# Performance work log

Hardware: AMD Instinct MI355X
Metric: run time of the kernel (lower is better)

The kernel has to match this reference:

```python
import math
import jax, jax.numpy as jnp
import numpy as np

NUM_HEADS = 32
KV_HEADS = 8
HEAD_DIM = 128
BLOCK_SIZE = 16
MAX_CTX = 2048
BSZ = 64
BLOCKS_PER_SEQ = MAX_CTX // BLOCK_SIZE  # 128
NUM_BLOCKS = BSZ * BLOCKS_PER_SEQ       # 8192


def setup_inputs() -> dict:
    key = jax.random.key(0)
    k1, k2, k3, k4 = jax.random.split(key, 4)
    query = jax.random.normal(k1, (BSZ, NUM_HEADS, HEAD_DIM), dtype=jnp.float32)
    key_cache = jax.random.normal(k2, (NUM_BLOCKS, KV_HEADS, BLOCK_SIZE, HEAD_DIM), dtype=jnp.float32)
    value_cache = jax.random.normal(k3, (NUM_BLOCKS, KV_HEADS, BLOCK_SIZE, HEAD_DIM), dtype=jnp.float32)
    # each sequence owns a contiguous run of blocks (valid paged layout)
    block_tables = jnp.arange(NUM_BLOCKS, dtype=jnp.int32).reshape(BSZ, BLOCKS_PER_SEQ)
    # per-sequence context lengths in [1, MAX_CTX]
    input_lens = jax.random.randint(k4, (BSZ,), 1, MAX_CTX + 1, dtype=jnp.int32)
    return {
        "query": query,
        "key_cache": key_cache,
        "value_cache": value_cache,
        "block_tables": block_tables,
        "input_lens": input_lens,
    }


def reference(query, key_cache, value_cache, block_tables, input_lens):
    """Paged single-query cached-KV attention with GQA (decode path of _IPEXAttention).

    query:       [bsz, num_heads, head_dim]  (one new token per sequence)
    key_cache:   [num_blocks, kv_heads, block_size, head_dim]
    value_cache: [num_blocks, kv_heads, block_size, head_dim]
    block_tables:[bsz, blocks_per_seq] int32
    input_lens:  [bsz] int32 valid context length per sequence
    returns:     [bsz, num_heads * head_dim]
    """
    bsz, nh, hd = query.shape
    groups = nh // KV_HEADS  # kv_head_mapping = arange(KV_HEADS).repeat_interleave(groups)
    scale = 1.0 / math.sqrt(hd)

    # Gather paged KV: [bsz, blocks, kvh, bs, hd] -> [bsz, kvh, S, hd]
    k = key_cache[block_tables].transpose(0, 2, 1, 3, 4).reshape(bsz, KV_HEADS, -1, hd)
    v = value_cache[block_tables].transpose(0, 2, 1, 3, 4).reshape(bsz, KV_HEADS, -1, hd)
    S = k.shape[2]

    # GQA: query heads grouped by their kv head
    q = query.reshape(bsz, KV_HEADS, groups, hd)

    scores = jnp.einsum("bkgd,bksd->bkgs", q, k) * scale  # [bsz, kvh, groups, S]
    valid = jnp.arange(S, dtype=jnp.int32)[None, :] < input_lens[:, None]  # [bsz, S]
    neg = jnp.finfo(scores.dtype).min
    scores = jnp.where(valid[:, None, None, :], scores, neg)
    probs = jax.nn.softmax(scores, axis=-1)

    out = jnp.einsum("bkgs,bksd->bkgd", probs, v)  # [bsz, kvh, groups, hd]
    # attn_output.reshape(-1, num_heads * head_dim) as in the torch module
    return out.reshape(bsz, nh * hd)
```

## Files before the change

### kernel.cpp

```cpp
#include <hip/hip_runtime.h>
#include <math.h>

#define NUM_HEADS 32
#define KV_HEADS 8
#define GROUPS 4
#define HEAD_DIM 128
#define BLOCK_SIZE 16
#define MAX_CTX 2048
#define BSZ 64
#define BLOCKS_PER_SEQ 128

#define CHUNK_BLOCKS 16
#define CHUNK_TOKENS (CHUNK_BLOCKS * BLOCK_SIZE)
#define NCHUNK (MAX_CTX / CHUNK_TOKENS)
#define REC_STRIDE 520

__global__ __launch_bounds__(256, 4)
void attn_partial_kernel(const float* __restrict__ q,
                         const float* __restrict__ kcache,
                         const float* __restrict__ vcache,
                         const int*   __restrict__ btab,
                         const int*   __restrict__ lens,
                         float*       __restrict__ part)
{
    const int chunk = blockIdx.x;
    const int kvh   = blockIdx.y;
    const int seq   = blockIdx.z;

    const int len  = lens[seq];
    const int tok0 = chunk * CHUNK_TOKENS;
    if (tok0 >= len) return;

    const int tid  = threadIdx.x;
    const int wave = tid >> 6;
    const int lane = tid & 63;
    const int half = lane >> 5;
    const int c    = lane & 31;

    const float scale = 0.08838834764831845f;

    float4 qv[GROUPS];
    const float* qbase = q + ((size_t)seq * NUM_HEADS + (size_t)kvh * GROUPS) * HEAD_DIM + c * 4;
#pragma unroll
    for (int h = 0; h < GROUPS; ++h) {
        float4 t = *(const float4*)(qbase + h * HEAD_DIM);
        qv[h] = make_float4(t.x * scale, t.y * scale, t.z * scale, t.w * scale);
    }

    float  m[GROUPS], l[GROUPS];
    float4 o[GROUPS];
#pragma unroll
    for (int h = 0; h < GROUPS; ++h) {
        m[h] = -INFINITY; l[h] = 0.f; o[h] = make_float4(0.f, 0.f, 0.f, 0.f);
    }

    const int nblk   = (len + BLOCK_SIZE - 1) / BLOCK_SIZE;
    const int bstart = chunk * CHUNK_BLOCKS;
    const int bend   = min(bstart + CHUNK_BLOCKS, nblk);

    for (int b = bstart + wave; b < bend; b += 4) {
        const int phys = btab[seq * BLOCKS_PER_SEQ + b];
        const size_t slice = ((size_t)phys * KV_HEADS + kvh) * (BLOCK_SIZE * HEAD_DIM);
        const float* kblk = kcache + slice;
        const float* vblk = vcache + slice;
        const int tbase = b * BLOCK_SIZE;

#pragma unroll
        for (int it = 0; it < 8; ++it) {
            const int off = (it * 64 + lane) * 4;
            float4 k4 = *(const float4*)(kblk + off);
            float4 v4 = *(const float4*)(vblk + off);
            const bool valid = (tbase + 2 * it + half) < len;

            float s[GROUPS];
#pragma unroll
            for (int h = 0; h < GROUPS; ++h) {
                float p = k4.x * qv[h].x + k4.y * qv[h].y + k4.z * qv[h].z + k4.w * qv[h].w;
#pragma unroll
                for (int d = 1; d < 32; d <<= 1)
                    p += __shfl_xor(p, d, 64);
                s[h] = p;
            }

            if (valid) {
#pragma unroll
                for (int h = 0; h < GROUPS; ++h) {
                    float mn    = fmaxf(m[h], s[h]);
                    float alpha = __expf(m[h] - mn);
                    float p     = __expf(s[h] - mn);
                    l[h] = l[h] * alpha + p;
                    o[h].x = o[h].x * alpha + p * v4.x;
                    o[h].y = o[h].y * alpha + p * v4.y;
                    o[h].z = o[h].z * alpha + p * v4.z;
                    o[h].w = o[h].w * alpha + p * v4.w;
                    m[h] = mn;
                }
            }
        }
    }

#pragma unroll
    for (int h = 0; h < GROUPS; ++h) {
        float mo = __shfl_xor(m[h], 32, 64);
        float m2 = fmaxf(m[h], mo);
        float w  = (m[h] == -INFINITY) ? 0.f : __expf(m[h] - m2);
        float ls = l[h] * w;
        l[h] = ls + __shfl_xor(ls, 32, 64);
        o[h].x *= w; o[h].y *= w; o[h].z *= w; o[h].w *= w;
        o[h].x += __shfl_xor(o[h].x, 32, 64);
        o[h].y += __shfl_xor(o[h].y, 32, 64);
        o[h].z += __shfl_xor(o[h].z, 32, 64);
        o[h].w += __shfl_xor(o[h].w, 32, 64);
        m[h] = m2;
    }

    __shared__ float o_lds[4][GROUPS][HEAD_DIM];
    __shared__ float m_lds[4][GROUPS];
    __shared__ float l_lds[4][GROUPS];
    if (half == 0) {
#pragma unroll
        for (int h = 0; h < GROUPS; ++h)
            *(float4*)&o_lds[wave][h][c * 4] = o[h];
        if (c == 0) {
#pragma unroll
            for (int h = 0; h < GROUPS; ++h) { m_lds[wave][h] = m[h]; l_lds[wave][h] = l[h]; }
        }
    }
    __syncthreads();

    float* rec = part + (((size_t)(seq * KV_HEADS + kvh)) * NCHUNK + chunk) * REC_STRIDE;
#pragma unroll
    for (int r = 0; r < 2; ++r) {
        const int e = tid + r * 256;
        const int h = e >> 7;
        const int d = e & 127;
        float mstar = fmaxf(fmaxf(m_lds[0][h], m_lds[1][h]),
                            fmaxf(m_lds[2][h], m_lds[3][h]));
        float num = 0.f, L = 0.f;
#pragma unroll
        for (int w = 0; w < 4; ++w) {
            float mw = m_lds[w][h];
            float ww = (mw == -INFINITY) ? 0.f : __expf(mw - mstar);
            num += o_lds[w][h][d] * ww;
            L   += l_lds[w][h] * ww;
        }
        rec[e] = num;
        if (d == 0) { rec[512 + h] = mstar; rec[516 + h] = L; }
    }
}

__global__ __launch_bounds__(256)
void attn_reduce_kernel(const float* __restrict__ part,
                        const int*   __restrict__ lens,
                        float*       __restrict__ out)
{
    const int kvh = blockIdx.x & (KV_HEADS - 1);
    const int seq = blockIdx.x / KV_HEADS;
    const int len = lens[seq];
    const int nlive = (len + CHUNK_TOKENS - 1) / CHUNK_TOKENS;

    const float* base = part + ((size_t)(seq * KV_HEADS + kvh)) * NCHUNK * REC_STRIDE;
    const int tid = threadIdx.x;

#pragma unroll
    for (int r = 0; r < 2; ++r) {
        const int e = tid + r * 256;
        const int h = e >> 7;
        const int d = e & 127;

        float mstar = -INFINITY;
        for (int ch = 0; ch < nlive; ++ch)
            mstar = fmaxf(mstar, base[ch * REC_STRIDE + 512 + h]);

        float num = 0.f, L = 0.f;
        for (int ch = 0; ch < nlive; ++ch) {
            const float* r0 = base + ch * REC_STRIDE;
            float ww = __expf(r0[512 + h] - mstar);
            num += r0[e] * ww;
            L   += r0[516 + h] * ww;
        }
        out[(size_t)seq * (NUM_HEADS * HEAD_DIM) + (kvh * GROUPS + h) * HEAD_DIM + d] = num / L;
    }
}

extern "C" void kernel_launch(void* const* d_in, const int* in_sizes, int n_in,
                              void* d_out, int out_size, void* d_ws, size_t ws_size,
                              hipStream_t stream) {
    const float* q    = (const float*)d_in[0];
    const float* kc   = (const float*)d_in[1];
    const float* vc   = (const float*)d_in[2];
    const int*   bt   = (const int*)d_in[3];
    const int*   lens = (const int*)d_in[4];
    float* out  = (float*)d_out;
    float* part = (float*)d_ws;

    dim3 g1(NCHUNK, KV_HEADS, BSZ);
    attn_partial_kernel<<<g1, 256, 0, stream>>>(q, kc, vc, bt, lens, part);

    dim3 g2(BSZ * KV_HEADS);
    attn_reduce_kernel<<<g2, 256, 0, stream>>>(part, lens, out);
}
```

Measured before the change: 991.9 us.

## Restructure decode attention per-block: 16-lane token groups, block-wise online softmax, exp2

Each wave now maps 16 lanes per token, with each lane covering 8 dims in two float4 halves, so a 16-token block is processed as 4 tokens per lane group. Shuffle reductions drop from 5 steps to 4 and are batched across 4 tokens and 4 heads. The online softmax rescale happens once per block instead of once per token. The log2e factor is folded into the query scale so exp2f can be used. This raises register pressure (launch bounds lowered to 3 blocks per SM) in exchange for fewer cross-lane ops and exp evaluations.

```diff
diff --git a/kernel.cpp b/kernel.cpp
--- a/kernel.cpp
+++ b/kernel.cpp
@@ -15,7 +15,7 @@
 #define NCHUNK (MAX_CTX / CHUNK_TOKENS)
 #define REC_STRIDE 520
 
-__global__ __launch_bounds__(256, 4)
+__global__ __launch_bounds__(256, 3)
 void attn_partial_kernel(const float* __restrict__ q,
                          const float* __restrict__ kcache,
                          const float* __restrict__ vcache,
@@ -27,31 +27,34 @@
     const int kvh   = blockIdx.y;
     const int seq   = blockIdx.z;
 
-    const int len  = lens[seq];
-    const int tok0 = chunk * CHUNK_TOKENS;
-    if (tok0 >= len) return;
+    const int len = lens[seq];
+    if (chunk * CHUNK_TOKENS >= len) return;
 
     const int tid  = threadIdx.x;
     const int wave = tid >> 6;
     const int lane = tid & 63;
-    const int half = lane >> 5;
-    const int c    = lane & 31;
-
-    const float scale = 0.08838834764831845f;
-
-    float4 qv[GROUPS];
-    const float* qbase = q + ((size_t)seq * NUM_HEADS + (size_t)kvh * GROUPS) * HEAD_DIM + c * 4;
+    const int g    = lane >> 4;
+    const int u    = lane & 15;
+
+    const float qs = 0.08838834764831845f * 1.44269504088896340736f;
+
+    float4 qa[GROUPS], qb[GROUPS];
+    const float* qbase = q + ((size_t)seq * NUM_HEADS + (size_t)kvh * GROUPS) * HEAD_DIM;
 #pragma unroll
     for (int h = 0; h < GROUPS; ++h) {
-        float4 t = *(const float4*)(qbase + h * HEAD_DIM);
-        qv[h] = make_float4(t.x * scale, t.y * scale, t.z * scale, t.w * scale);
+        float4 t = *(const float4*)(qbase + h * HEAD_DIM + 4 * u);
+        qa[h] = make_float4(t.x * qs, t.y * qs, t.z * qs, t.w * qs);
+        t = *(const float4*)(qbase + h * HEAD_DIM + 64 + 4 * u);
+        qb[h] = make_float4(t.x * qs, t.y * qs, t.z * qs, t.w * qs);
     }
 
     float  m[GROUPS], l[GROUPS];
-    float4 o[GROUPS];
+    float4 oa[GROUPS], ob[GROUPS];
 #pragma unroll
     for (int h = 0; h < GROUPS; ++h) {
-        m[h] = -INFINITY; l[h] = 0.f; o[h] = make_float4(0.f, 0.f, 0.f, 0.f);
+        m[h] = -INFINITY; l[h] = 0.f;
+        oa[h] = make_float4(0.f, 0.f, 0.f, 0.f);
+        ob[h] = make_float4(0.f, 0.f, 0.f, 0.f);
     }
 
     const int nblk   = (len + BLOCK_SIZE - 1) / BLOCK_SIZE;
@@ -63,65 +66,101 @@
         const size_t slice = ((size_t)phys * KV_HEADS + kvh) * (BLOCK_SIZE * HEAD_DIM);
         const float* kblk = kcache + slice;
         const float* vblk = vcache + slice;
-        const int tbase = b * BLOCK_SIZE;
-
-#pragma unroll
-        for (int it = 0; it < 8; ++it) {
-            const int off = (it * 64 + lane) * 4;
-            float4 k4 = *(const float4*)(kblk + off);
-            float4 v4 = *(const float4*)(vblk + off);
-            const bool valid = (tbase + 2 * it + half) < len;
-
-            float s[GROUPS];
+
+        float  s[4][GROUPS];
+        float4 va[4], vb[4];
+#pragma unroll
+        for (int j = 0; j < 4; ++j) {
+            const int off = (4 * j + g) * HEAD_DIM + 4 * u;
+            float4 ka = *(const float4*)(kblk + off);
+            float4 kb = *(const float4*)(kblk + off + 64);
+            va[j] = *(const float4*)(vblk + off);
+            vb[j] = *(const float4*)(vblk + off + 64);
 #pragma unroll
             for (int h = 0; h < GROUPS; ++h) {
-                float p = k4.x * qv[h].x + k4.y * qv[h].y + k4.z * qv[h].z + k4.w * qv[h].w;
-#pragma unroll
-                for (int d = 1; d < 32; d <<= 1)
-                    p += __shfl_xor(p, d, 64);
-                s[h] = p;
+                s[j][h] = ka.x * qa[h].x + ka.y * qa[h].y + ka.z * qa[h].z + ka.w * qa[h].w
+                        + kb.x * qb[h].x + kb.y * qb[h].y + kb.z * qb[h].z + kb.w * qb[h].w;
             }
-
-            if (valid) {
-#pragma unroll
-                for (int h = 0; h < GROUPS; ++h) {
-                    float mn    = fmaxf(m[h], s[h]);
-                    float alpha = __expf(m[h] - mn);
-                    float p     = __expf(s[h] - mn);
-                    l[h] = l[h] * alpha + p;
-                    o[h].x = o[h].x * alpha + p * v4.x;
-                    o[h].y = o[h].y * alpha + p * v4.y;
-                    o[h].z = o[h].z * alpha + p * v4.z;
-                    o[h].w = o[h].w * alpha + p * v4.w;
-                    m[h] = mn;
-                }
+        }
+
+#pragma unroll
+        for (int d = 1; d < 16; d <<= 1) {
+#pragma unroll
+            for (int j = 0; j < 4; ++j)
+#pragma unroll
+                for (int h = 0; h < GROUPS; ++h)
+                    s[j][h] += __shfl_xor(s[j][h], d, 64);
+        }
+
+        const int tb = b * BLOCK_SIZE + g;
+#pragma unroll
+        for (int j = 0; j < 4; ++j) {
+            if (tb + 4 * j >= len) {
+#pragma unroll
+                for (int h = 0; h < GROUPS; ++h) s[j][h] = -INFINITY;
             }
         }
-    }
-
-#pragma unroll
-    for (int h = 0; h < GROUPS; ++h) {
-        float mo = __shfl_xor(m[h], 32, 64);
-        float m2 = fmaxf(m[h], mo);
-        float w  = (m[h] == -INFINITY) ? 0.f : __expf(m[h] - m2);
-        float ls = l[h] * w;
-        l[h] = ls + __shfl_xor(ls, 32, 64);
-        o[h].x *= w; o[h].y *= w; o[h].z *= w; o[h].w *= w;
-        o[h].x += __shfl_xor(o[h].x, 32, 64);
-        o[h].y += __shfl_xor(o[h].y, 32, 64);
-        o[h].z += __shfl_xor(o[h].z, 32, 64);
-        o[h].w += __shfl_xor(o[h].w, 32, 64);
-        m[h] = m2;
+
+#pragma unroll
+        for (int h = 0; h < GROUPS; ++h) {
+            float bm = fmaxf(fmaxf(s[0][h], s[1][h]), fmaxf(s[2][h], s[3][h]));
+            bm = fmaxf(bm, __shfl_xor(bm, 16, 64));
+            bm = fmaxf(bm, __shfl_xor(bm, 32, 64));
+            const float mn    = fmaxf(m[h], bm);
+            const float alpha = exp2f(m[h] - mn);
+            l[h] *= alpha;
+            oa[h].x *= alpha; oa[h].y *= alpha; oa[h].z *= alpha; oa[h].w *= alpha;
+            ob[h].x *= alpha; ob[h].y *= alpha; ob[h].z *= alpha; ob[h].w *= alpha;
+            m[h] = mn;
+        }
+
+#pragma unroll
+        for (int j = 0; j < 4; ++j) {
+#pragma unroll
+            for (int h = 0; h < GROUPS; ++h) {
+                const float p = exp2f(s[j][h] - m[h]);
+                l[h] += p;
+                oa[h].x += p * va[j].x; oa[h].y += p * va[j].y;
+                oa[h].z += p * va[j].z; oa[h].w += p * va[j].w;
+                ob[h].x += p * vb[j].x; ob[h].y += p * vb[j].y;
+                ob[h].z += p * vb[j].z; ob[h].w += p * vb[j].w;
+            }
+        }
+    }
+
+#pragma unroll
+    for (int d = 16; d <= 32; d <<= 1) {
+#pragma unroll
+        for (int h = 0; h < GROUPS; ++h) {
+            const float mo = __shfl_xor(m[h], d, 64);
+            const float mn = fmaxf(m[h], mo);
+            const float w  = (m[h] == -INFINITY) ? 0.f : exp2f(m[h] - mn);
+            float ls = l[h] * w;
+            l[h] = ls + __shfl_xor(ls, d, 64);
+            oa[h].x *= w; oa[h].y *= w; oa[h].z *= w; oa[h].w *= w;
+            ob[h].x *= w; ob[h].y *= w; ob[h].z *= w; ob[h].w *= w;
+            oa[h].x += __shfl_xor(oa[h].x, d, 64);
+            oa[h].y += __shfl_xor(oa[h].y, d, 64);
+            oa[h].z += __shfl_xor(oa[h].z, d, 64);
+            oa[h].w += __shfl_xor(oa[h].w, d, 64);
+            ob[h].x += __shfl_xor(ob[h].x, d, 64);
+            ob[h].y += __shfl_xor(ob[h].y, d, 64);
+            ob[h].z += __shfl_xor(ob[h].z, d, 64);
+            ob[h].w += __shfl_xor(ob[h].w, d, 64);
+            m[h] = mn;
+        }
     }
 
     __shared__ float o_lds[4][GROUPS][HEAD_DIM];
     __shared__ float m_lds[4][GROUPS];
     __shared__ float l_lds[4][GROUPS];
-    if (half == 0) {
-#pragma unroll
-        for (int h = 0; h < GROUPS; ++h)
-            *(float4*)&o_lds[wave][h][c * 4] = o[h];
-        if (c == 0) {
+    if (g == 0) {
+#pragma unroll
+        for (int h = 0; h < GROUPS; ++h) {
+            *(float4*)&o_lds[wave][h][4 * u]      = oa[h];
+            *(float4*)&o_lds[wave][h][64 + 4 * u] = ob[h];
+        }
+        if (u == 0) {
 #pragma unroll
             for (int h = 0; h < GROUPS; ++h) { m_lds[wave][h] = m[h]; l_lds[wave][h] = l[h]; }
         }
@@ -140,7 +179,7 @@
 #pragma unroll
         for (int w = 0; w < 4; ++w) {
             float mw = m_lds[w][h];
-            float ww = (mw == -INFINITY) ? 0.f : __expf(mw - mstar);
+            float ww = (mw == -INFINITY) ? 0.f : exp2f(mw - mstar);
             num += o_lds[w][h][d] * ww;
             L   += l_lds[w][h] * ww;
         }
@@ -175,7 +214,7 @@
         float num = 0.f, L = 0.f;
         for (int ch = 0; ch < nlive; ++ch) {
             const float* r0 = base + ch * REC_STRIDE;
-            float ww = __expf(r0[512 + h] - mstar);
+            float ww = exp2f(r0[512 + h] - mstar);
             num += r0[e] * ww;
             L   += r0[516 + h] * ww;
         }
```

Result: faster. 939.6 us (-5.3%).
